# Performance work log

Measured on AMD Instinct MI355X. Metric: run time of the kernel, lower is better.

Reference implementation:

```python
import jax, jax.numpy as jnp
import numpy as np
from jax import lax

C = 4; ITERS = 3; WIN = 5; SIGMA = 0.5
B, H, W = 2, 256, 256


def conv2d(x, w, b=None, pad=1, dil=1, groups=1):
    y = lax.conv_general_dilated(x, w, (1, 1), [(pad, pad), (pad, pad)],
                                 rhs_dilation=(dil, dil),
                                 dimension_numbers=("NCHW", "OIHW", "NCHW"),
                                 feature_group_count=groups)
    if b is not None:
        y = y + b[None, :, None, None]
    return y


def _sobel_kernels():
    kx = np.array([[-1, 0, 1], [-2, 0, 2], [-1, 0, 1]], np.float32)
    ky = np.array([[-1, -2, -1], [0, 0, 0], [1, 2, 1]], np.float32)
    kx = np.tile(kx[None, None], (C, 1, 1, 1))
    ky = np.tile(ky[None, None], (C, 1, 1, 1))
    return jnp.asarray(kx), jnp.asarray(ky)


_BOX = jnp.ones((C, 1, WIN, WIN), jnp.float32)


def boxsum(x):
    # depthwise 5x5 ones conv == sum over the unfold window (same math as F.unfold + sum)
    return conv2d(x, _BOX, pad=WIN // 2, groups=C)


def _grad_mag(state, kx, ky):
    gx = conv2d(state, kx, pad=1, groups=C)
    gy = conv2d(state, ky, pad=1, groups=C)
    return jnp.sqrt(gx * gx + gy * gy)


def _forward(x, target_modality, fc_w, fc_b, modality_w,
             su_w1, su_b1, su_w2, su_b2, nu_w1, nu_b1, nu_w2, nu_b2,
             dc_w, dc_b, sobel_kx, sobel_ky):
    # input gating
    gfeat = jnp.mean(x, axis=(2, 3))                                   # (B,C) global avg pool
    in_w = jax.nn.sigmoid(gfeat @ fc_w.T + fc_b)[:, :, None, None]
    state = x * in_w * jax.nn.sigmoid(modality_w)[None, :, None, None]
    for _ in range(ITERS):
        upd = conv2d(jax.nn.relu(conv2d(state, su_w1, su_b1, pad=1)), su_w2, su_b2, pad=1)
        nbr = conv2d(jax.nn.relu(conv2d(state, nu_w1, nu_b1, pad=2, dil=2)), nu_w2, nu_b2, pad=2, dil=2)
        gm = _grad_mag(state, sobel_kx, sobel_ky)
        # dist[p] = sum_k (gm_patch_k - gm[p])^2; expand the square -> box sums (identical math
        # to the torch unfold version, which sums over the window dim producing a per-pixel scalar)
        dist = boxsum(gm * gm) - 2.0 * gm * boxsum(gm) + float(WIN * WIN) * gm * gm
        sim = jnp.exp(-dist / (2.0 * SIGMA * SIGMA))
        sim = sim / (jnp.sum(sim, axis=(2, 3), keepdims=True) + 1e-8)  # normalized over H*W per (b,c)
        weighted = sim * boxsum(state)                                 # sim broadcasts over the window sum
        hf = conv2d(state, dc_w, dc_b, pad=1)                          # DynamicConv (assumed Conv2d C->C, k=3)
        state = weighted + upd + nbr + hf
    # positive/negative sample weights, per-sample branch selected by target_modality
    gm = _grad_mag(state, sobel_kx, sobel_ky)
    sgm = jax.nn.sigmoid(gm)
    hf = jax.nn.sigmoid(conv2d(state, dc_w, dc_b, pad=1))
    pos_br = jnp.stack([hf, sgm, hf * sgm, jax.nn.sigmoid(gm * hf)], 0)            # (4,B,C,H,W)
    neg_br = jnp.stack([1 - sgm, 1 - hf, 1 - hf * sgm, 1 - jax.nn.sigmoid(gm * hf)], 0)
    bidx = jnp.arange(x.shape[0])
    pos = jnp.clip(pos_br[target_modality, bidx], 0.0, 1.0)
    neg = jnp.clip(neg_br[target_modality, bidx], 0.0, 1.0)
    sel = jnp.exp(pos) / (jnp.exp(pos) + jnp.exp(neg) + 1e-8)
    # ContrastiveLoss is not defined in the source; simple surrogate (see notes)
    loss = jnp.mean(sel * neg + (1.0 - sel) * pos)
    return state * sel, loss


def setup_inputs() -> dict:
    key = jax.random.key(0)
    ks = jax.random.split(key, 10)
    sobel_kx, sobel_ky = _sobel_kernels()
    s = 0.05
    return dict(
        x=jax.random.normal(ks[0], (B, C, H, W), jnp.float32),
        target_modality=jax.random.randint(ks[1], (B,), 0, C),
        fc_w=jax.random.normal(ks[2], (C, C), jnp.float32) * 0.1,
        fc_b=jnp.zeros((C,), jnp.float32),
        modality_w=jnp.ones((C,), jnp.float32),
        su_w1=jax.random.normal(ks[3], (128, C, 3, 3), jnp.float32) * s,
        su_b1=jnp.zeros((128,), jnp.float32),
        su_w2=jax.random.normal(ks[4], (C, 128, 3, 3), jnp.float32) * s,
        su_b2=jnp.zeros((C,), jnp.float32),
        nu_w1=jax.random.normal(ks[5], (128, C, 3, 3), jnp.float32) * s,
        nu_b1=jnp.zeros((128,), jnp.float32),
        nu_w2=jax.random.normal(ks[6], (C, 128, 3, 3), jnp.float32) * s,
        nu_b2=jnp.zeros((C,), jnp.float32),
        dc_w=jax.random.normal(ks[7], (C, C, 3, 3), jnp.float32) * s,
        dc_b=jnp.zeros((C,), jnp.float32),
        sobel_kx=sobel_kx,
        sobel_ky=sobel_ky,
    )


def reference(x, target_modality, fc_w, fc_b, modality_w,
              su_w1, su_b1, su_w2, su_b2, nu_w1, nu_b1, nu_w2, nu_b2,
              dc_w, dc_b, sobel_kx, sobel_ky):
    return _forward(x, target_modality, fc_w, fc_b, modality_w,
                    su_w1, su_b1, su_w2, su_b2, nu_w1, nu_b1, nu_w2, nu_b2,
                    dc_w, dc_b, sobel_kx, sobel_ky)
```

## Files before the change

### kernel.cpp

```cpp
#include <hip/hip_runtime.h>
#include <math.h>

#define HW 256
#define NPIX (HW*HW)
#define TOT (2*4*NPIX)

__device__ __forceinline__ float sigmoidf_(float v) { return 1.f / (1.f + expf(-v)); }

__global__ __launch_bounds__(256) void k_gfeat(const float* __restrict__ x, float* __restrict__ gfeat) {
    int bc = blockIdx.x;
    const float* p = x + (size_t)bc * NPIX;
    float s = 0.f;
    for (int i = threadIdx.x; i < NPIX; i += 256) s += p[i];
    for (int off = 32; off; off >>= 1) s += __shfl_down(s, off);
    __shared__ float ls[4];
    if ((threadIdx.x & 63) == 0) ls[threadIdx.x >> 6] = s;
    __syncthreads();
    if (threadIdx.x == 0) gfeat[bc] = (ls[0] + ls[1] + ls[2] + ls[3]) / (float)NPIX;
}

__global__ __launch_bounds__(256) void k_gate(const float* __restrict__ x,
        const float* __restrict__ gfeat, const float* __restrict__ fc_w,
        const float* __restrict__ fc_b, const float* __restrict__ mw,
        float* __restrict__ state) {
    int idx = blockIdx.x * 256 + threadIdx.x;
    int c = (idx >> 16) & 3, b = idx >> 18;
    float a = fc_b[c];
#pragma unroll
    for (int j = 0; j < 4; ++j) a = fmaf(gfeat[b*4+j], fc_w[c*4+j], a);
    float s = sigmoidf_(a) * sigmoidf_(mw[c]);
    state[idx] = x[idx] * s;
}

template<int D>
__global__ __launch_bounds__(256, 4) void branch_conv(const float* __restrict__ state,
        const float* __restrict__ w1, const float* __restrict__ b1,
        const float* __restrict__ w2, const float* __restrict__ b2,
        float* __restrict__ out) {
    constexpr int T1 = 16 + 2*D;
    constexpr int TP = T1 + 2;
    constexpr int S  = 16 + 4*D;
    constexpr int SP = S + 1;
    __shared__ float s_state[4][S][SP];
    __shared__ float s_t1[16][T1][TP];

    const int half = blockIdx.z & 1;
    const int b    = blockIdx.z >> 1;
    const int ty0 = blockIdx.y * 16, tx0 = blockIdx.x * 16;
    const int tid = threadIdx.x;

    for (int i = tid; i < 4 * S * S; i += 256) {
        int ic = i / (S*S); int r = i % (S*S); int sy = r / S; int sx = r % S;
        int Y = ty0 - 2*D + sy, X = tx0 - 2*D + sx;
        float v = 0.f;
        if (Y >= 0 && Y < HW && X >= 0 && X < HW)
            v = state[((b*4 + ic) * NPIX) + Y*HW + X];
        s_state[ic][sy][sx] = v;
    }

    const int iy = tid >> 4, ix = tid & 15;
    float acc[4];
#pragma unroll
    for (int oc = 0; oc < 4; ++oc) acc[oc] = (half == 0) ? b2[oc] : 0.f;

    for (int ch = 0; ch < 4; ++ch) {
        __syncthreads();
        for (int e = tid; e < T1*T1; e += 256) {
            int ly = e / T1, lx = e - ly*T1;
            int Y = ty0 - D + ly, X = tx0 - D + lx;
            bool valid = (Y >= 0 && Y < HW && X >= 0 && X < HW);
            float patch[36];
#pragma unroll
            for (int ic = 0; ic < 4; ++ic)
#pragma unroll
                for (int dy = 0; dy < 3; ++dy)
#pragma unroll
                    for (int dx = 0; dx < 3; ++dx)
                        patch[ic*9 + dy*3 + dx] = s_state[ic][ly + dy*D][lx + dx*D];
#pragma unroll
            for (int o = 0; o < 16; ++o) {
                int goc = half*64 + ch*16 + o;
                const float* wr = &w1[goc*36];
                float a = b1[goc];
#pragma unroll
                for (int k = 0; k < 36; ++k) a = fmaf(patch[k], wr[k], a);
                s_t1[o][ly][lx] = valid ? fmaxf(a, 0.f) : 0.f;
            }
        }
        __syncthreads();
#pragma unroll
        for (int icl = 0; icl < 16; ++icl) {
            float t[9];
#pragma unroll
            for (int dy = 0; dy < 3; ++dy)
#pragma unroll
                for (int dx = 0; dx < 3; ++dx)
                    t[dy*3+dx] = s_t1[icl][iy + dy*D][ix + dx*D];
            int gic = half*64 + ch*16 + icl;
#pragma unroll
            for (int oc = 0; oc < 4; ++oc) {
                const float* wr = &w2[(oc*128 + gic)*9];
#pragma unroll
                for (int k = 0; k < 9; ++k) acc[oc] = fmaf(t[k], wr[k], acc[oc]);
            }
        }
    }
    float* op = out + (size_t)half * TOT;
#pragma unroll
    for (int oc = 0; oc < 4; ++oc)
        op[((b*4 + oc) * NPIX) + (ty0 + iy)*HW + (tx0 + ix)] = acc[oc];
}

__global__ __launch_bounds__(256) void k_sim(const float* __restrict__ state,
        float* __restrict__ sim, float* __restrict__ bs_state_o, float* __restrict__ sums) {
    const int bc = blockIdx.z;
    const int ty0 = blockIdx.y * 32, tx0 = blockIdx.x * 32;
    const float* sp = state + (size_t)bc * NPIX;
    __shared__ float st[38][38];
    __shared__ float gmt[36][36];
    __shared__ float rs_g[36][32], rs_g2[36][32], rs_s[36][32];
    const int tid = threadIdx.x;

    for (int i = tid; i < 38*38; i += 256) {
        int sy = i / 38, sx = i % 38;
        int Y = ty0 - 3 + sy, X = tx0 - 3 + sx;
        float v = 0.f;
        if (Y >= 0 && Y < HW && X >= 0 && X < HW) v = sp[Y*HW + X];
        st[sy][sx] = v;
    }
    __syncthreads();
    for (int i = tid; i < 36*36; i += 256) {
        int ly = i / 36, lx = i % 36;
        int Y = ty0 - 2 + ly, X = tx0 - 2 + lx;
        float g = 0.f;
        if (Y >= 0 && Y < HW && X >= 0 && X < HW) {
            float a00 = st[ly][lx],   a01 = st[ly][lx+1],   a02 = st[ly][lx+2];
            float a10 = st[ly+1][lx],                       a12 = st[ly+1][lx+2];
            float a20 = st[ly+2][lx], a21 = st[ly+2][lx+1], a22 = st[ly+2][lx+2];
            float gx = (a02 + 2.f*a12 + a22) - (a00 + 2.f*a10 + a20);
            float gy = (a20 + 2.f*a21 + a22) - (a00 + 2.f*a01 + a02);
            g = sqrtf(gx*gx + gy*gy);
        }
        gmt[ly][lx] = g;
    }
    __syncthreads();
    for (int i = tid; i < 36*32; i += 256) {
        int ly = i / 32, ix = i % 32;
        float sg = 0.f, sg2 = 0.f, ss = 0.f;
#pragma unroll
        for (int d = 0; d < 5; ++d) {
            float g = gmt[ly][ix + d];
            sg += g; sg2 += g*g;
            ss += st[ly + 1][ix + d + 1];
        }
        rs_g[ly][ix] = sg; rs_g2[ly][ix] = sg2; rs_s[ly][ix] = ss;
    }
    __syncthreads();
    float lsum = 0.f;
#pragma unroll
    for (int k = 0; k < 4; ++k) {
        int i = tid + k*256;
        int iy = i >> 5, ix = i & 31;
        float bg = 0.f, bg2 = 0.f, bs = 0.f;
#pragma unroll
        for (int d = 0; d < 5; ++d) { bg += rs_g[iy+d][ix]; bg2 += rs_g2[iy+d][ix]; bs += rs_s[iy+d][ix]; }
        float g = gmt[iy+2][ix+2];
        float dist = bg2 - 2.f*g*bg + 25.f*g*g;
        float sv = expf(-2.f * dist);
        int gi = bc*NPIX + (ty0+iy)*HW + (tx0+ix);
        sim[gi] = sv;
        bs_state_o[gi] = bs;
        lsum += sv;
    }
    for (int off = 32; off; off >>= 1) lsum += __shfl_down(lsum, off);
    __shared__ float ls[4];
    if ((tid & 63) == 0) ls[tid >> 6] = lsum;
    __syncthreads();
    if (tid == 0) atomicAdd(&sums[bc], ls[0] + ls[1] + ls[2] + ls[3]);
}

__global__ __launch_bounds__(256) void k_combine(const float* __restrict__ state,
        const float* __restrict__ sim, const float* __restrict__ bs_state,
        const float* __restrict__ upd, const float* __restrict__ nbr,
        const float* __restrict__ dc_w, const float* __restrict__ dc_b,
        const float* __restrict__ sums, float* __restrict__ state_out) {
    int idx = blockIdx.x * 256 + threadIdx.x;
    int x = idx & 255, y = (idx >> 8) & 255, c = (idx >> 16) & 3, b = idx >> 18;
    float hf = dc_b[c];
#pragma unroll
    for (int ic = 0; ic < 4; ++ic) {
        const float* sp = state + ((b*4 + ic) * NPIX);
#pragma unroll
        for (int dy = -1; dy <= 1; ++dy)
#pragma unroll
            for (int dx = -1; dx <= 1; ++dx) {
                int Y = y + dy, X = x + dx;
                float v = (Y >= 0 && Y < HW && X >= 0 && X < HW) ? sp[Y*HW + X] : 0.f;
                hf = fmaf(v, dc_w[((c*4 + ic)*3 + dy + 1)*3 + dx + 1], hf);
            }
    }
    float w = sim[idx] / (sums[b*4 + c] + 1e-8f) * bs_state[idx];
    state_out[idx] = w + (upd[idx] + upd[idx + TOT]) + (nbr[idx] + nbr[idx + TOT]) + hf;
}

__global__ __launch_bounds__(256) void k_epilogue(const float* __restrict__ state,
        const int* __restrict__ tm, const float* __restrict__ dc_w, const float* __restrict__ dc_b,
        float* __restrict__ out, float* __restrict__ loss_acc) {
    int idx = blockIdx.x * 256 + threadIdx.x;
    int x = idx & 255, y = (idx >> 8) & 255, c = (idx >> 16) & 3, b = idx >> 18;
    const float* sp = state + ((b*4 + c) * NPIX);
    float a00, a01, a02, a10, a12, a20, a21, a22;
    {
        auto rd = [&](int Y, int X) -> float {
            return (Y >= 0 && Y < HW && X >= 0 && X < HW) ? sp[Y*HW + X] : 0.f;
        };
        a00 = rd(y-1,x-1); a01 = rd(y-1,x); a02 = rd(y-1,x+1);
        a10 = rd(y,  x-1);                  a12 = rd(y,  x+1);
        a20 = rd(y+1,x-1); a21 = rd(y+1,x); a22 = rd(y+1,x+1);
    }
    float gx = (a02 + 2.f*a12 + a22) - (a00 + 2.f*a10 + a20);
    float gy = (a20 + 2.f*a21 + a22) - (a00 + 2.f*a01 + a02);
    float gm = sqrtf(gx*gx + gy*gy);
    float hfl = dc_b[c];
#pragma unroll
    for (int ic = 0; ic < 4; ++ic) {
        const float* sp2 = state + ((b*4 + ic) * NPIX);
#pragma unroll
        for (int dy = -1; dy <= 1; ++dy)
#pragma unroll
            for (int dx = -1; dx <= 1; ++dx) {
                int Y = y + dy, X = x + dx;
                float v = (Y >= 0 && Y < HW && X >= 0 && X < HW) ? sp2[Y*HW + X] : 0.f;
                hfl = fmaf(v, dc_w[((c*4 + ic)*3 + dy + 1)*3 + dx + 1], hfl);
            }
    }
    float hf = sigmoidf_(hfl);
    float sgm = sigmoidf_(gm);
    int t = tm[b];
    float pos, neg;
    if (t == 0)      { pos = hf;                      neg = 1.f - sgm; }
    else if (t == 1) { pos = sgm;                     neg = 1.f - hf; }
    else if (t == 2) { pos = hf * sgm;                neg = 1.f - hf * sgm; }
    else             { float q = sigmoidf_(gm * hf);  pos = q;  neg = 1.f - q; }
    pos = fminf(fmaxf(pos, 0.f), 1.f);
    neg = fminf(fmaxf(neg, 0.f), 1.f);
    float ep = expf(pos), en = expf(neg);
    float sel = ep / (ep + en + 1e-8f);
    out[idx] = sp[y*HW + x] * sel;
    float lt = sel * neg + (1.f - sel) * pos;
    for (int off = 32; off; off >>= 1) lt += __shfl_down(lt, off);
    __shared__ float ls[4];
    if ((threadIdx.x & 63) == 0) ls[threadIdx.x >> 6] = lt;
    __syncthreads();
    if (threadIdx.x == 0) atomicAdd(loss_acc, ls[0] + ls[1] + ls[2] + ls[3]);
}

__global__ void k_write_loss(const float* __restrict__ loss, float* __restrict__ out) {
    out[TOT] = loss[0] / (float)TOT;
}

extern "C" void kernel_launch(void* const* d_in, const int* in_sizes, int n_in,
                              void* d_out, int out_size, void* d_ws, size_t ws_size,
                              hipStream_t stream) {
    const float* x     = (const float*)d_in[0];
    const int*   tm    = (const int*)  d_in[1];
    const float* fc_w  = (const float*)d_in[2];
    const float* fc_b  = (const float*)d_in[3];
    const float* mw    = (const float*)d_in[4];
    const float* su_w1 = (const float*)d_in[5];
    const float* su_b1 = (const float*)d_in[6];
    const float* su_w2 = (const float*)d_in[7];
    const float* su_b2 = (const float*)d_in[8];
    const float* nu_w1 = (const float*)d_in[9];
    const float* nu_b1 = (const float*)d_in[10];
    const float* nu_w2 = (const float*)d_in[11];
    const float* nu_b2 = (const float*)d_in[12];
    const float* dc_w  = (const float*)d_in[13];
    const float* dc_b  = (const float*)d_in[14];

    float* ws      = (float*)d_ws;
    float* state_a = ws;
    float* state_b = ws + (size_t)TOT;
    float* upd     = ws + (size_t)2*TOT;
    float* nbr     = ws + (size_t)4*TOT;
    float* sim     = ws + (size_t)6*TOT;
    float* bs      = ws + (size_t)7*TOT;
    float* gfeat   = ws + (size_t)8*TOT;
    float* sums    = gfeat + 8;
    float* loss    = sums + 24;

    hipMemsetAsync(sums, 0, 25 * sizeof(float), stream);
    k_gfeat<<<8, 256, 0, stream>>>(x, gfeat);
    k_gate<<<TOT/256, 256, 0, stream>>>(x, gfeat, fc_w, fc_b, mw, state_a);

    float* cur = state_a; float* nxt = state_b;
    dim3 gbc(16, 16, 4);
    dim3 g32(8, 8, 8);
    for (int it = 0; it < 3; ++it) {
        branch_conv<1><<<gbc, 256, 0, stream>>>(cur, su_w1, su_b1, su_w2, su_b2, upd);
        branch_conv<2><<<gbc, 256, 0, stream>>>(cur, nu_w1, nu_b1, nu_w2, nu_b2, nbr);
        k_sim<<<g32, 256, 0, stream>>>(cur, sim, bs, sums + it*8);
        k_combine<<<TOT/256, 256, 0, stream>>>(cur, sim, bs, upd, nbr, dc_w, dc_b, sums + it*8, nxt);
        float* t = cur; cur = nxt; nxt = t;
    }
    k_epilogue<<<TOT/256, 256, 0, stream>>>(cur, tm, dc_w, dc_b, (float*)d_out, loss);
    k_write_loss<<<1, 1, 0, stream>>>(loss, (float*)d_out);
}
```

Measured before the change: 896.3 us.

## Split fused branch conv into two kernels via global 128-channel intermediate

The fused branch_conv, which recomputes the 128-channel hidden activation on halo tiles in shared memory, is replaced by two kernels. The first writes the ReLU'd 128-channel intermediate to a global workspace, and the second reads it back to compute the 4-channel output, split across two halves. This removes redundant halo recomputation and large shared memory use, which may raise occupancy. In exchange it writes and reads about 64 MB of intermediate per branch per iteration, and it only takes this path when the workspace is large enough.

```diff
diff --git a/kernel.cpp b/kernel.cpp
--- a/kernel.cpp
+++ b/kernel.cpp
@@ -30,6 +30,113 @@
     for (int j = 0; j < 4; ++j) a = fmaf(gfeat[b*4+j], fc_w[c*4+j], a);
     float s = sigmoidf_(a) * sigmoidf_(mw[c]);
     state[idx] = x[idx] * s;
+}
+
+template<int D>
+__global__ __launch_bounds__(256) void k_conv1(const float* __restrict__ state,
+        const float* __restrict__ w1, const float* __restrict__ b1,
+        float* __restrict__ t1) {
+    constexpr int S = 16 + 2*D;
+    constexpr int SP = S + 1;
+    __shared__ float s_state[4][S][SP];
+    const int oh = blockIdx.z & 1;
+    const int b  = blockIdx.z >> 1;
+    const int ty0 = blockIdx.y * 16, tx0 = blockIdx.x * 16;
+    const int tid = threadIdx.x;
+
+    for (int i = tid; i < 4*S*S; i += 256) {
+        int ic = i / (S*S); int r = i % (S*S); int sy = r / S; int sx = r % S;
+        int Y = ty0 - D + sy, X = tx0 - D + sx;
+        float v = 0.f;
+        if (Y >= 0 && Y < HW && X >= 0 && X < HW)
+            v = state[((b*4 + ic) * NPIX) + Y*HW + X];
+        s_state[ic][sy][sx] = v;
+    }
+    __syncthreads();
+
+    const int iy = tid >> 4, ix = tid & 15;
+    float patch[36];
+#pragma unroll
+    for (int ic = 0; ic < 4; ++ic)
+#pragma unroll
+        for (int dy = 0; dy < 3; ++dy)
+#pragma unroll
+            for (int dx = 0; dx < 3; ++dx)
+                patch[ic*9 + dy*3 + dx] = s_state[ic][iy + dy*D][ix + dx*D];
+
+    float* op = t1 + ((size_t)b * 128 * NPIX) + (ty0 + iy)*HW + (tx0 + ix);
+    for (int ocq = 0; ocq < 16; ++ocq) {
+        const int oc = oh*64 + ocq*4;
+        const float* wr = &w1[oc*36];
+        float a0 = b1[oc], a1 = b1[oc+1], a2 = b1[oc+2], a3 = b1[oc+3];
+#pragma unroll
+        for (int k = 0; k < 36; ++k) {
+            float p = patch[k];
+            a0 = fmaf(p, wr[k],       a0);
+            a1 = fmaf(p, wr[36 + k],  a1);
+            a2 = fmaf(p, wr[72 + k],  a2);
+            a3 = fmaf(p, wr[108 + k], a3);
+        }
+        op[(size_t)(oc+0)*NPIX] = fmaxf(a0, 0.f);
+        op[(size_t)(oc+1)*NPIX] = fmaxf(a1, 0.f);
+        op[(size_t)(oc+2)*NPIX] = fmaxf(a2, 0.f);
+        op[(size_t)(oc+3)*NPIX] = fmaxf(a3, 0.f);
+    }
+}
+
+template<int D>
+__global__ __launch_bounds__(256) void k_conv2(const float* __restrict__ t1,
+        const float* __restrict__ w2, const float* __restrict__ b2,
+        float* __restrict__ out) {
+    constexpr int T = 16 + 2*D;
+    constexpr int TP = T + 2;
+    __shared__ float s_t[16][T][TP];
+    const int half = blockIdx.z & 1;
+    const int b    = blockIdx.z >> 1;
+    const int ty0 = blockIdx.y * 16, tx0 = blockIdx.x * 16;
+    const int tid = threadIdx.x;
+    const int iy = tid >> 4, ix = tid & 15;
+
+    float acc0, acc1, acc2, acc3;
+    if (half == 0) { acc0 = b2[0]; acc1 = b2[1]; acc2 = b2[2]; acc3 = b2[3]; }
+    else           { acc0 = acc1 = acc2 = acc3 = 0.f; }
+
+    for (int ch = 0; ch < 4; ++ch) {
+        __syncthreads();
+        for (int icl = 0; icl < 16; ++icl) {
+            const float* gp = t1 + ((size_t)(b*128 + half*64 + ch*16 + icl) * NPIX);
+            for (int j = tid; j < T*T; j += 256) {
+                int r = j / T, c = j - r*T;
+                int Y = ty0 - D + r, X = tx0 - D + c;
+                float v = 0.f;
+                if (Y >= 0 && Y < HW && X >= 0 && X < HW) v = gp[Y*HW + X];
+                s_t[icl][r][c] = v;
+            }
+        }
+        __syncthreads();
+#pragma unroll 4
+        for (int icl = 0; icl < 16; ++icl) {
+            int gic = half*64 + ch*16 + icl;
+            const float* wr0 = &w2[(0*128 + gic)*9];
+            const float* wr1 = &w2[(1*128 + gic)*9];
+            const float* wr2 = &w2[(2*128 + gic)*9];
+            const float* wr3 = &w2[(3*128 + gic)*9];
+#pragma unroll
+            for (int dy = 0; dy < 3; ++dy)
+#pragma unroll
+                for (int dx = 0; dx < 3; ++dx) {
+                    float tv = s_t[icl][iy + dy*D][ix + dx*D];
+                    int k = dy*3 + dx;
+                    acc0 = fmaf(tv, wr0[k], acc0);
+                    acc1 = fmaf(tv, wr1[k], acc1);
+                    acc2 = fmaf(tv, wr2[k], acc2);
+                    acc3 = fmaf(tv, wr3[k], acc3);
+                }
+        }
+    }
+    float* op = out + (size_t)half * TOT;
+    size_t o = ((size_t)(b*4)) * NPIX + (ty0 + iy)*HW + (tx0 + ix);
+    op[o] = acc0; op[o + NPIX] = acc1; op[o + 2*NPIX] = acc2; op[o + 3*NPIX] = acc3;
 }
 
 template<int D>
@@ -285,20 +392,33 @@
     float* nbr     = ws + (size_t)4*TOT;
     float* sim     = ws + (size_t)6*TOT;
     float* bs      = ws + (size_t)7*TOT;
-    float* gfeat   = ws + (size_t)8*TOT;
-    float* sums    = gfeat + 8;
-    float* loss    = sums + 24;
+
+    const size_t need_fast = ((size_t)40*TOT + 64) * sizeof(float);
+    const bool fast = (ws_size >= need_fast);
+
+    float* t1    = ws + (size_t)8*TOT;
+    float* small = fast ? (ws + (size_t)40*TOT) : (ws + (size_t)8*TOT);
+    float* gfeat = small;
+    float* sums  = small + 8;
+    float* loss  = sums + 24;
 
     hipMemsetAsync(sums, 0, 25 * sizeof(float), stream);
     k_gfeat<<<8, 256, 0, stream>>>(x, gfeat);
     k_gate<<<TOT/256, 256, 0, stream>>>(x, gfeat, fc_w, fc_b, mw, state_a);
 
     float* cur = state_a; float* nxt = state_b;
-    dim3 gbc(16, 16, 4);
+    dim3 g4(16, 16, 4);
     dim3 g32(8, 8, 8);
     for (int it = 0; it < 3; ++it) {
-        branch_conv<1><<<gbc, 256, 0, stream>>>(cur, su_w1, su_b1, su_w2, su_b2, upd);
-        branch_conv<2><<<gbc, 256, 0, stream>>>(cur, nu_w1, nu_b1, nu_w2, nu_b2, nbr);
+        if (fast) {
+            k_conv1<1><<<g4, 256, 0, stream>>>(cur, su_w1, su_b1, t1);
+            k_conv2<1><<<g4, 256, 0, stream>>>(t1, su_w2, su_b2, upd);
+            k_conv1<2><<<g4, 256, 0, stream>>>(cur, nu_w1, nu_b1, t1);
+            k_conv2<2><<<g4, 256, 0, stream>>>(t1, nu_w2, nu_b2, nbr);
+        } else {
+            branch_conv<1><<<g4, 256, 0, stream>>>(cur, su_w1, su_b1, su_w2, su_b2, upd);
+            branch_conv<2><<<g4, 256, 0, stream>>>(cur, nu_w1, nu_b1, nu_w2, nu_b2, nbr);
+        }
         k_sim<<<g32, 256, 0, stream>>>(cur, sim, bs, sums + it*8);
         k_combine<<<TOT/256, 256, 0, stream>>>(cur, sim, bs, upd, nbr, dc_w, dc_b, sums + it*8, nxt);
         float* t = cur; cur = nxt; nxt = t;
```

New measurement: 1.056 ms. 17.8% more time.
